# Kernel optimization log

Measured on AMD Instinct MI355X. Metric: run time of the kernel, lower is better.

Reference implementation:

```python
import jax, jax.numpy as jnp
import numpy as np

N_UE = 100000
N_AP = 10000
N_E = 1600000
D = 64
H = 128


def setup_inputs() -> dict:
    key = jax.random.key(0)
    ks = jax.random.split(key, 10)
    s = 0.05
    return {
        "ue_hid": jax.random.normal(ks[0], (N_UE, D), jnp.float32),
        "ap_hid": jax.random.normal(ks[1], (N_AP, D), jnp.float32),
        "edge_hid": jax.random.normal(ks[2], (N_E, D), jnp.float32),
        "src": jax.random.randint(ks[3], (N_E,), 0, N_UE),
        "dst": jax.random.randint(ks[4], (N_E,), 0, N_AP),
        "W1a": jax.random.normal(ks[5], (2 * D, H), jnp.float32) * s,
        "b1a": jnp.zeros((H,), jnp.float32),
        "W1b": jax.random.normal(ks[6], (H, H), jnp.float32) * s,
        "b1b": jnp.zeros((H,), jnp.float32),
        "W2a": jax.random.normal(ks[7], (D + H, H), jnp.float32) * s,
        "b2a": jnp.zeros((H,), jnp.float32),
        "W2b": jax.random.normal(ks[8], (H, D), jnp.float32) * s,
        "b2b": jnp.zeros((D,), jnp.float32),
    }


def reference(ue_hid, ap_hid, edge_hid, src, dst,
              W1a, b1a, W1b, b1b, W2a, b2a, W2b, b2b):
    # message: concat(edge_feature, src UE feature) -> [E, 2D]
    msg = jnp.concatenate([edge_hid, ue_hid[src]], axis=-1)
    # mlp1 applied per edge (DGL applies it inside reduce on the mailbox,
    # which is equivalent to per-edge application followed by segment sum)
    h = jnp.maximum(msg @ W1a + b1a, 0.0) @ W1b + b1b          # [E, H]
    # sum over mailbox (all edges with the same destination AP)
    agg = jax.ops.segment_sum(h, dst, num_segments=N_AP)        # [N_AP, H]
    # mlp2 on concat(AP hid, aggregated messages)
    z = jnp.concatenate([ap_hid, agg], axis=-1)                 # [N_AP, D+H]
    new_ap = jnp.maximum(z @ W2a + b2a, 0.0) @ W2b + b2b        # [N_AP, D]
    return new_ap
```

## Files before the change

kernel.cpp:

```cpp
#include <hip/hip_runtime.h>
#include <hip/hip_bf16.h>

#define N_UE 100000
#define N_AP 10000
#define N_E  1600000
#define DD   64
#define HH   128
#define NTILE (N_E / 128)

typedef float f32x4 __attribute__((ext_vector_type(4)));
typedef short s8b   __attribute__((ext_vector_type(8)));
typedef short s4b   __attribute__((ext_vector_type(4)));

static __device__ __forceinline__ unsigned short f2bf(float x) {
  union { float f; unsigned int u; } v; v.f = x;
  unsigned int r = v.u + 0x7fffu + ((v.u >> 16) & 1u);
  return (unsigned short)(r >> 16);
}

__global__ void apk0_prep(const float* __restrict__ W1a, short* __restrict__ WTg,
                          int* __restrict__ counts, float* __restrict__ aggW) {
  int i = blockIdx.x * 256 + threadIdx.x;
  int n = gridDim.x * 256;
  for (int x = i; x < 128 * 128; x += n) {
    int col = x >> 7, k = x & 127;
    WTg[x] = (short)f2bf(W1a[k * 128 + col]);
  }
  for (int x = i; x < N_AP; x += n) counts[x] = 0;
  for (int x = i; x < N_AP * 128 / 4; x += n)
    ((float4*)aggW)[x] = make_float4(0.f, 0.f, 0.f, 0.f);
}

__global__ void apk2_hist(const int* __restrict__ dst, int* __restrict__ counts) {
  int i = blockIdx.x * blockDim.x + threadIdx.x;
  int stride = gridDim.x * blockDim.x;
  for (; i < N_E; i += stride) atomicAdd(&counts[dst[i]], 1);
}

__global__ __launch_bounds__(256) void apk3_scan(const int* __restrict__ counts,
                                                 int* __restrict__ offsets,
                                                 int* __restrict__ cursor) {
  __shared__ int p[256];
  int t = threadIdx.x;
  const int CH = 40;
  int start = t * CH, end = min(start + CH, N_AP);
  int s = 0;
  for (int i = start; i < end; i++) s += counts[i];
  p[t] = s;
  __syncthreads();
  for (int d = 1; d < 256; d <<= 1) {
    int v = p[t] + ((t >= d) ? p[t - d] : 0);
    __syncthreads();
    p[t] = v;
    __syncthreads();
  }
  int base = (t == 0) ? 0 : p[t - 1];
  for (int i = start; i < end; i++) {
    offsets[i] = base;
    cursor[i] = base;
    base += counts[i];
  }
  if (t == 255) offsets[N_AP] = base;
}

__global__ void apk4_scatter(const int* __restrict__ dst, const int* __restrict__ src,
                             int* __restrict__ cursor, int4* __restrict__ triple) {
  int i = blockIdx.x * blockDim.x + threadIdx.x;
  int stride = gridDim.x * blockDim.x;
  for (; i < N_E; i += stride) {
    int d = dst[i];
    int pos = atomicAdd(&cursor[d], 1);
    triple[pos] = make_int4(i, src[i], d, 0);
  }
}

__global__ __launch_bounds__(256, 4) void apk5_edges(
    const float* __restrict__ edge_hid, const float* __restrict__ ue_hid,
    const short* __restrict__ WTg, const float* __restrict__ b1a,
    const int4* __restrict__ triple, float* __restrict__ aggW) {
  __shared__ short A[128][132];
  __shared__ int segs[128];
  int t = threadIdx.x;
  int wave = t >> 6, lane = t & 63, quad = lane >> 4, l16 = lane & 15;

  s8b bf[2][4];
  for (int ct = 0; ct < 2; ct++)
    for (int ks = 0; ks < 4; ks++)
      bf[ct][ks] = *(const s8b*)&WTg[(wave * 32 + ct * 16 + l16) * 128 +
                                     ks * 32 + quad * 8];
  float bias0 = b1a[wave * 32 + l16];
  float bias1 = b1a[wave * 32 + 16 + l16];

  int runseg = -1;
  float run0 = 0.f, run1 = 0.f;
  auto flush = [&]() {
    if (runseg >= 0) {
      float f0 = run0 + __shfl_xor(run0, 16); f0 += __shfl_xor(f0, 32);
      float f1 = run1 + __shfl_xor(run1, 16); f1 += __shfl_xor(f1, 32);
      if (quad == 0) {
        atomicAdd(&aggW[(size_t)runseg * 128 + wave * 32 + l16], f0);
        atomicAdd(&aggW[(size_t)runseg * 128 + wave * 32 + 16 + l16], f1);
      }
    }
  };

  const int r = t >> 1, h = t & 1;
  for (int tile = blockIdx.x; tile < NTILE; tile += gridDim.x) {
    int4 tr = triple[(size_t)tile * 128 + r];
    __syncthreads();
    if (h == 0) segs[r] = tr.z;
    {
      const float* srow = h ? (ue_hid + (size_t)tr.y * 64)
                            : (edge_hid + (size_t)tr.x * 64);
      int kb = h * 64;
      #pragma unroll
      for (int cc = 0; cc < 8; cc++) {
        float4 v = ((const float4*)srow)[cc * 2];
        float4 w = ((const float4*)srow)[cc * 2 + 1];
        s8b p;
        p[0] = (short)f2bf(v.x); p[1] = (short)f2bf(v.y);
        p[2] = (short)f2bf(v.z); p[3] = (short)f2bf(v.w);
        p[4] = (short)f2bf(w.x); p[5] = (short)f2bf(w.y);
        p[6] = (short)f2bf(w.z); p[7] = (short)f2bf(w.w);
        *(s8b*)&A[r][kb + cc * 8] = p;
      }
    }
    __syncthreads();

    for (int rt = 0; rt < 8; rt++) {
      s8b a0 = *(const s8b*)&A[rt * 16 + l16][0 + quad * 8];
      s8b a1 = *(const s8b*)&A[rt * 16 + l16][32 + quad * 8];
      s8b a2 = *(const s8b*)&A[rt * 16 + l16][64 + quad * 8];
      s8b a3 = *(const s8b*)&A[rt * 16 + l16][96 + quad * 8];
      f32x4 c0 = {0.f, 0.f, 0.f, 0.f}, c1 = {0.f, 0.f, 0.f, 0.f};
      c0 = __builtin_amdgcn_mfma_f32_16x16x32_bf16(a0, bf[0][0], c0, 0, 0, 0);
      c0 = __builtin_amdgcn_mfma_f32_16x16x32_bf16(a1, bf[0][1], c0, 0, 0, 0);
      c0 = __builtin_amdgcn_mfma_f32_16x16x32_bf16(a2, bf[0][2], c0, 0, 0, 0);
      c0 = __builtin_amdgcn_mfma_f32_16x16x32_bf16(a3, bf[0][3], c0, 0, 0, 0);
      c1 = __builtin_amdgcn_mfma_f32_16x16x32_bf16(a0, bf[1][0], c1, 0, 0, 0);
      c1 = __builtin_amdgcn_mfma_f32_16x16x32_bf16(a1, bf[1][1], c1, 0, 0, 0);
      c1 = __builtin_amdgcn_mfma_f32_16x16x32_bf16(a2, bf[1][2], c1, 0, 0, 0);
      c1 = __builtin_amdgcn_mfma_f32_16x16x32_bf16(a3, bf[1][3], c1, 0, 0, 0);
      float t0[4], t1[4];
      #pragma unroll
      for (int j = 0; j < 4; j++) {
        t0[j] = fmaxf(c0[j] + bias0, 0.f);
        t1[j] = fmaxf(c1[j] + bias1, 0.f);
      }
      int gb = rt * 16;
      int sF = segs[gb], sL = segs[gb + 15];
      if (sF == sL) {
        if (sF != runseg) { flush(); runseg = sF; run0 = 0.f; run1 = 0.f; }
        run0 += t0[0] + t0[1] + t0[2] + t0[3];
        run1 += t1[0] + t1[1] + t1[2] + t1[3];
      } else {
        int sj[4];
        #pragma unroll
        for (int j = 0; j < 4; j++) sj[j] = segs[gb + quad * 4 + j];
        for (int s = sF; s <= sL; s++) {
          float v0 = 0.f, v1 = 0.f;
          #pragma unroll
          for (int j = 0; j < 4; j++)
            if (sj[j] == s) { v0 += t0[j]; v1 += t1[j]; }
          if (s == runseg) { run0 += v0; run1 += v1; }
          else { flush(); runseg = s; run0 = v0; run1 = v1; }
        }
      }
    }
  }
  flush();
}

__global__ __launch_bounds__(256) void apk6_mlp2(
    const float* __restrict__ ap_hid, const float* __restrict__ W1b,
    const float* __restrict__ b1b, const float* __restrict__ W2a,
    const float* __restrict__ b2a, const float* __restrict__ W2b,
    const float* __restrict__ b2b, const float* __restrict__ aggW,
    const int* __restrict__ offsets, float* __restrict__ out) {
  __shared__ float wbuf[64 * 128];
  __shared__ float zrows[16 * 128];
  __shared__ float yrows[16 * 128];
  __shared__ float arows[16 * 64];
  __shared__ float cbuf[16];
  int t = threadIdx.x;
  int apb = blockIdx.x * 16;
  for (int i = t; i < 16 * 128 / 4; i += 256)
    ((float4*)zrows)[i] = ((const float4*)(aggW + (size_t)apb * 128))[i];
  for (int i = t; i < 16 * 64 / 4; i += 256)
    ((float4*)arows)[i] = ((const float4*)(ap_hid + (size_t)apb * 64))[i];
  if (t < 16) cbuf[t] = (float)(offsets[apb + t + 1] - offsets[apb + t]);
  int j = t & 127, half = t >> 7;
  {
    float bb = b1b[j];
    __syncthreads();
    float acc[8];
    for (int r = 0; r < 8; r++) acc[r] = cbuf[half * 8 + r] * bb;
    for (int p = 0; p < 2; p++) {
      __syncthreads();
      for (int i = t; i < 64 * 128 / 4; i += 256)
        ((float4*)wbuf)[i] = ((const float4*)(W1b + p * 64 * 128))[i];
      __syncthreads();
      for (int k = 0; k < 64; k++) {
        float w = wbuf[k * 128 + j];
        for (int r = 0; r < 8; r++)
          acc[r] += zrows[(half * 8 + r) * 128 + (p * 64 + k)] * w;
      }
    }
    for (int r = 0; r < 8; r++) yrows[(half * 8 + r) * 128 + j] = acc[r];
  }
  {
    float acc2[8];
    float bb = b2a[j];
    for (int r = 0; r < 8; r++) acc2[r] = bb;
    __syncthreads();
    for (int i = t; i < 64 * 128 / 4; i += 256)
      ((float4*)wbuf)[i] = ((const float4*)W2a)[i];
    __syncthreads();
    for (int k = 0; k < 64; k++) {
      float w = wbuf[k * 128 + j];
      for (int r = 0; r < 8; r++) acc2[r] += arows[(half * 8 + r) * 64 + k] * w;
    }
    for (int p = 0; p < 2; p++) {
      __syncthreads();
      for (int i = t; i < 64 * 128 / 4; i += 256)
        ((float4*)wbuf)[i] = ((const float4*)(W2a + (64 + p * 64) * 128))[i];
      __syncthreads();
      for (int k = 0; k < 64; k++) {
        float w = wbuf[k * 128 + j];
        for (int r = 0; r < 8; r++)
          acc2[r] += yrows[(half * 8 + r) * 128 + (p * 64 + k)] * w;
      }
    }
    __syncthreads();
    for (int r = 0; r < 8; r++)
      zrows[(half * 8 + r) * 128 + j] = fmaxf(acc2[r], 0.f);
  }
  {
    __syncthreads();
    for (int i = t; i < 128 * 64 / 4; i += 256)
      ((float4*)wbuf)[i] = ((const float4*)W2b)[i];
    __syncthreads();
    int i2 = t & 63, q = t >> 6;
    float acc3[4];
    float bb = b2b[i2];
    for (int r = 0; r < 4; r++) acc3[r] = bb;
    for (int k = 0; k < 128; k++) {
      float w = wbuf[k * 64 + i2];
      for (int r = 0; r < 4; r++) acc3[r] += zrows[(q * 4 + r) * 128 + k] * w;
    }
    for (int r = 0; r < 4; r++)
      out[(size_t)(apb + q * 4 + r) * 64 + i2] = acc3[r];
  }
}

extern "C" void kernel_launch(void* const* d_in, const int* in_sizes, int n_in,
                              void* d_out, int out_size, void* d_ws, size_t ws_size,
                              hipStream_t stream) {
  const float* ue_hid   = (const float*)d_in[0];
  const float* ap_hid   = (const float*)d_in[1];
  const float* edge_hid = (const float*)d_in[2];
  const int*   src      = (const int*)d_in[3];
  const int*   dst      = (const int*)d_in[4];
  const float* W1a      = (const float*)d_in[5];
  const float* b1a      = (const float*)d_in[6];
  const float* W1b      = (const float*)d_in[7];
  const float* b1b      = (const float*)d_in[8];
  const float* W2a      = (const float*)d_in[9];
  const float* b2a      = (const float*)d_in[10];
  const float* W2b      = (const float*)d_in[11];
  const float* b2b      = (const float*)d_in[12];
  float* out = (float*)d_out;

  unsigned char* ws = (unsigned char*)d_ws;
  short* WTg    = (short*)(ws);
  int* counts   = (int*)(ws + 32768);
  int* offsets  = (int*)(ws + 73728);
  int* cursor   = (int*)(ws + 114688);
  float* aggW   = (float*)(ws + 155648);
  int4* triple  = (int4*)(ws + 5275648);

  apk0_prep<<<640, 256, 0, stream>>>(W1a, WTg, counts, aggW);
  apk2_hist<<<2048, 256, 0, stream>>>(dst, counts);
  apk3_scan<<<1, 256, 0, stream>>>(counts, offsets, cursor);
  apk4_scatter<<<2048, 256, 0, stream>>>(dst, src, cursor, triple);
  apk5_edges<<<2048, 256, 0, stream>>>(edge_hid, ue_hid, WTg, b1a, triple, aggW);
  apk6_mlp2<<<N_AP / 16, 256, 0, stream>>>(ap_hid, W1b, b1b, W2a, b2a, W2b, b2b,
                                           aggW, offsets, out);
}
```

Measured before the change: 914.3 us.

## Software-pipeline edge-tile gathers with double-buffered LDS and register prefetch

The edge kernel now prefetches the next tile's triple and gathered feature rows into registers while the current tile's MFMA work runs, using double-buffered shared memory for the bf16 A tile and segment IDs. One barrier per tile is removed. The float-to-bf16 conversion now packs pairs with a byte-permute instead of per-element rounding. The grid drops to 512 blocks with occupancy hint 2, trading parallelism for latency hiding. The 64 float registers per thread raise register pressure.

Result: no change. 931.5 us (+1.9%).

```diff
diff --git a/kernel.cpp b/kernel.cpp
--- a/kernel.cpp
+++ b/kernel.cpp
@@ -7,15 +7,18 @@
 #define DD   64
 #define HH   128
 #define NTILE (N_E / 128)
+#define GRID5 512
 
 typedef float f32x4 __attribute__((ext_vector_type(4)));
 typedef short s8b   __attribute__((ext_vector_type(8)));
-typedef short s4b   __attribute__((ext_vector_type(4)));
 
 static __device__ __forceinline__ unsigned short f2bf(float x) {
   union { float f; unsigned int u; } v; v.f = x;
   unsigned int r = v.u + 0x7fffu + ((v.u >> 16) & 1u);
   return (unsigned short)(r >> 16);
+}
+static __device__ __forceinline__ unsigned int pk2(unsigned int lo, unsigned int hi) {
+  return __builtin_amdgcn_perm(hi + 0x8000u, lo + 0x8000u, 0x07060302u);
 }
 
 __global__ void apk0_prep(const float* __restrict__ W1a, short* __restrict__ WTg,
@@ -74,12 +77,12 @@
   }
 }
 
-__global__ __launch_bounds__(256, 4) void apk5_edges(
+__global__ __launch_bounds__(256, 2) void apk5_edges(
     const float* __restrict__ edge_hid, const float* __restrict__ ue_hid,
     const short* __restrict__ WTg, const float* __restrict__ b1a,
     const int4* __restrict__ triple, float* __restrict__ aggW) {
-  __shared__ short A[128][132];
-  __shared__ int segs[128];
+  __shared__ short A[2][128][132];
+  __shared__ int segs[2][128];
   int t = threadIdx.x;
   int wave = t >> 6, lane = t & 63, quad = lane >> 4, l16 = lane & 15;
 
@@ -105,33 +108,45 @@
   };
 
   const int r = t >> 1, h = t & 1;
-  for (int tile = blockIdx.x; tile < NTILE; tile += gridDim.x) {
-    int4 tr = triple[(size_t)tile * 128 + r];
-    __syncthreads();
-    if (h == 0) segs[r] = tr.z;
+  int tile = blockIdx.x;
+  int4 tr = triple[(size_t)tile * 128 + r];
+  float4 gv[16];
+  {
+    const float* srow = h ? (ue_hid + (size_t)tr.y * 64)
+                          : (edge_hid + (size_t)tr.x * 64);
+    #pragma unroll
+    for (int cc = 0; cc < 16; cc++) gv[cc] = ((const float4*)srow)[cc];
+  }
+  int nb = 0;
+  for (; tile < NTILE; tile += GRID5) {
+    int nxt = tile + GRID5;
+    if (nxt >= NTILE) nxt = blockIdx.x;
+    int4 trn = triple[(size_t)nxt * 128 + r];
+    if (h == 0) segs[nb][r] = tr.z;
+    #pragma unroll
+    for (int cc = 0; cc < 8; cc++) {
+      const unsigned int* d0 = (const unsigned int*)&gv[cc * 2];
+      const unsigned int* d1 = (const unsigned int*)&gv[cc * 2 + 1];
+      union { s8b s; unsigned int u[4]; } P;
+      P.u[0] = pk2(d0[0], d0[1]);
+      P.u[1] = pk2(d0[2], d0[3]);
+      P.u[2] = pk2(d1[0], d1[1]);
+      P.u[3] = pk2(d1[2], d1[3]);
+      *(s8b*)&A[nb][r][h * 64 + cc * 8] = P.s;
+    }
+    __syncthreads();
+    tr = trn;
     {
       const float* srow = h ? (ue_hid + (size_t)tr.y * 64)
                             : (edge_hid + (size_t)tr.x * 64);
-      int kb = h * 64;
       #pragma unroll
-      for (int cc = 0; cc < 8; cc++) {
-        float4 v = ((const float4*)srow)[cc * 2];
-        float4 w = ((const float4*)srow)[cc * 2 + 1];
-        s8b p;
-        p[0] = (short)f2bf(v.x); p[1] = (short)f2bf(v.y);
-        p[2] = (short)f2bf(v.z); p[3] = (short)f2bf(v.w);
-        p[4] = (short)f2bf(w.x); p[5] = (short)f2bf(w.y);
-        p[6] = (short)f2bf(w.z); p[7] = (short)f2bf(w.w);
-        *(s8b*)&A[r][kb + cc * 8] = p;
-      }
-    }
-    __syncthreads();
-
+      for (int cc = 0; cc < 16; cc++) gv[cc] = ((const float4*)srow)[cc];
+    }
     for (int rt = 0; rt < 8; rt++) {
-      s8b a0 = *(const s8b*)&A[rt * 16 + l16][0 + quad * 8];
-      s8b a1 = *(const s8b*)&A[rt * 16 + l16][32 + quad * 8];
-      s8b a2 = *(const s8b*)&A[rt * 16 + l16][64 + quad * 8];
-      s8b a3 = *(const s8b*)&A[rt * 16 + l16][96 + quad * 8];
+      s8b a0 = *(const s8b*)&A[nb][rt * 16 + l16][0 + quad * 8];
+      s8b a1 = *(const s8b*)&A[nb][rt * 16 + l16][32 + quad * 8];
+      s8b a2 = *(const s8b*)&A[nb][rt * 16 + l16][64 + quad * 8];
+      s8b a3 = *(const s8b*)&A[nb][rt * 16 + l16][96 + quad * 8];
       f32x4 c0 = {0.f, 0.f, 0.f, 0.f}, c1 = {0.f, 0.f, 0.f, 0.f};
       c0 = __builtin_amdgcn_mfma_f32_16x16x32_bf16(a0, bf[0][0], c0, 0, 0, 0);
       c0 = __builtin_amdgcn_mfma_f32_16x16x32_bf16(a1, bf[0][1], c0, 0, 0, 0);
@@ -148,7 +163,7 @@
         t1[j] = fmaxf(c1[j] + bias1, 0.f);
       }
       int gb = rt * 16;
-      int sF = segs[gb], sL = segs[gb + 15];
+      int sF = segs[nb][gb], sL = segs[nb][gb + 15];
       if (sF == sL) {
         if (sF != runseg) { flush(); runseg = sF; run0 = 0.f; run1 = 0.f; }
         run0 += t0[0] + t0[1] + t0[2] + t0[3];
@@ -156,7 +171,7 @@
       } else {
         int sj[4];
         #pragma unroll
-        for (int j = 0; j < 4; j++) sj[j] = segs[gb + quad * 4 + j];
+        for (int j = 0; j < 4; j++) sj[j] = segs[nb][gb + quad * 4 + j];
         for (int s = sF; s <= sL; s++) {
           float v0 = 0.f, v1 = 0.f;
           #pragma unroll
@@ -167,6 +182,7 @@
         }
       }
     }
+    nb ^= 1;
   }
   flush();
 }
@@ -283,7 +299,7 @@
   apk2_hist<<<2048, 256, 0, stream>>>(dst, counts);
   apk3_scan<<<1, 256, 0, stream>>>(counts, offsets, cursor);
   apk4_scatter<<<2048, 256, 0, stream>>>(dst, src, cursor, triple);
-  apk5_edges<<<2048, 256, 0, stream>>>(edge_hid, ue_hid, WTg, b1a, triple, aggW);
+  apk5_edges<<<GRID5, 256, 0, stream>>>(edge_hid, ue_hid, WTg, b1a, triple, aggW);
   apk6_mlp2<<<N_AP / 16, 256, 0, stream>>>(ap_hid, W1b, b1b, W2a, b2a, W2b, b2b,
                                            aggW, offsets, out);
 }
```
